# Performance work log

Measured on AMD Instinct MI355X. Metric: run time of the kernel, lower is better.

The kernel has to match this reference:

```python
import jax, jax.numpy as jnp
import numpy as np

NUM_HEADS = 8
NUM_GROUPS = 32
EPS = 1e-5


def group_norm(x, gamma, beta):
    # x: [B, C, H, W]; normalize over (C//G, H, W) within each of G groups
    B, C, H, W = x.shape
    xg = x.reshape(B, NUM_GROUPS, C // NUM_GROUPS, H, W)
    mean = xg.mean(axis=(2, 3, 4), keepdims=True)
    var = xg.var(axis=(2, 3, 4), keepdims=True)
    xn = ((xg - mean) * jax.lax.rsqrt(var + EPS)).reshape(B, C, H, W)
    return xn * gamma[None, :, None, None] + beta[None, :, None, None]


def setup_inputs() -> dict:
    key = jax.random.key(0)
    ks = jax.random.split(key, 7)
    B, C, H, W = 16, 512, 32, 32
    x = jax.random.normal(ks[0], (B, C, H, W), dtype=jnp.float32)
    gamma = jnp.ones((C,), dtype=jnp.float32)
    beta = jnp.zeros((C,), dtype=jnp.float32)
    # 1x1 convs == per-pixel linear layers
    w_qkv = jax.random.normal(ks[1], (3 * C, C), dtype=jnp.float32) * (1.0 / np.sqrt(C))
    b_qkv = jax.random.normal(ks[2], (3 * C,), dtype=jnp.float32) * 0.02
    w_proj = jax.random.normal(ks[3], (C, C), dtype=jnp.float32) * (1.0 / np.sqrt(C))
    b_proj = jax.random.normal(ks[4], (C,), dtype=jnp.float32) * 0.02
    return {"x": x, "gamma": gamma, "beta": beta, "w_qkv": w_qkv,
            "b_qkv": b_qkv, "w_proj": w_proj, "b_proj": b_proj}


def reference(x, gamma, beta, w_qkv, b_qkv, w_proj, b_proj):
    B, C, H, W = x.shape
    nh = NUM_HEADS
    d = C // nh
    N = H * W
    h = group_norm(x, gamma, beta)
    # 1x1 conv: [B,C,H,W] x [3C,C] -> [B,3C,H,W]
    qkv = jnp.einsum('bchw,oc->bohw', h, w_qkv) + b_qkv[None, :, None, None]
    qkv = qkv.reshape(B, 3, nh, d, N)  # matches torch reshape(B,3,heads,d,HW)
    q, k, v = qkv[:, 0], qkv[:, 1], qkv[:, 2]
    scale = d ** (-0.5)
    attn = jnp.einsum('bhdn,bhdm->bhnm', q, k) * scale  # [B,h,N,N]
    attn = jax.nn.softmax(attn, axis=-1)
    out = jnp.einsum('bhnm,bhdm->bhdn', attn, v)  # [B,h,d,N]
    out = out.reshape(B, C, H, W)
    proj = jnp.einsum('bchw,oc->bohw', out, w_proj) + b_proj[None, :, None, None]
    return x + proj
```

## Files before the change

kernel.cpp:

```cpp
#include <hip/hip_runtime.h>
#include <cstddef>

#define B_  16
#define C_  512
#define N_  1024

typedef __attribute__((ext_vector_type(8))) __bf16 bf16x8;
typedef __attribute__((ext_vector_type(4))) float f32x4;
typedef __attribute__((ext_vector_type(4))) short s16x4;

__device__ __forceinline__ unsigned short f2bf(float x) {
  unsigned u = __float_as_uint(x);
  return (unsigned short)((u + 0x7fffu + ((u >> 16) & 1u)) >> 16);
}
__device__ __forceinline__ float bf2f(unsigned short h) {
  return __uint_as_float(((unsigned)h) << 16);
}

#define GLDS16(g, l)                                                            \
  __builtin_amdgcn_global_load_lds(                                             \
      (const __attribute__((address_space(1))) void*)(g),                       \
      (__attribute__((address_space(3))) void*)(l), 16, 0, 0)

__global__ __launch_bounds__(256) void wconv_kernel(
    const float* __restrict__ wq, const float* __restrict__ wp,
    unsigned short* __restrict__ oq, unsigned short* __restrict__ op) {
  int i = blockIdx.x * 256 + threadIdx.x;
  const float4* src; unsigned short* dst; int off;
  if (i < 196608) { src = (const float4*)wq; dst = oq; off = i; }
  else            { src = (const float4*)wp; dst = op; off = i - 196608; }
  float4 v = src[off];
  union { unsigned short s[4]; ushort4 u; } o;
  o.s[0] = f2bf(v.x); o.s[1] = f2bf(v.y);
  o.s[2] = f2bf(v.z); o.s[3] = f2bf(v.w);
  *(ushort4*)(dst + (size_t)off * 4) = o.u;
}

__global__ __launch_bounds__(256) void gn_kernel(
    const float* __restrict__ x, const float* __restrict__ gamma,
    const float* __restrict__ beta, unsigned short* __restrict__ hT) {
  int bg = blockIdx.x;
  int b = bg >> 5, g = bg & 31;
  size_t base = ((size_t)b * C_ + (size_t)g * 16) * N_;
  const float4* x4 = (const float4*)(x + base);
  int tid = threadIdx.x;

  float sum = 0.f, sq = 0.f;
  float4 vv[16];
#pragma unroll
  for (int i = 0; i < 16; i++) {
    float4 v = x4[tid + i * 256];
    vv[i] = v;
    sum += v.x + v.y + v.z + v.w;
    sq  += v.x * v.x + v.y * v.y + v.z * v.z + v.w * v.w;
  }
#pragma unroll
  for (int off = 32; off > 0; off >>= 1) {
    sum += __shfl_down(sum, off, 64);
    sq  += __shfl_down(sq, off, 64);
  }
  __shared__ float sm[4], sv[4];
  int lane = tid & 63, w = tid >> 6;
  if (lane == 0) { sm[w] = sum; sv[w] = sq; }
  __syncthreads();
  if (tid == 0) {
    float s = sm[0] + sm[1] + sm[2] + sm[3];
    float q = sv[0] + sv[1] + sv[2] + sv[3];
    float mean = s * (1.f / 16384.f);
    float var  = q * (1.f / 16384.f) - mean * mean;
    sm[0] = mean;
    sv[0] = rsqrtf(var + 1e-5f);
  }
  __syncthreads();
  float mean = sm[0], rstd = sv[0];

  union { unsigned short s[16]; uint4 u[2]; } row[4];
#pragma unroll
  for (int i = 0; i < 16; i++) {
    int c = g * 16 + i;
    float ga = gamma[c] * rstd;
    float be = beta[c] - mean * ga;
    float4 v = vv[i];
    row[0].s[i] = f2bf(v.x * ga + be);
    row[1].s[i] = f2bf(v.y * ga + be);
    row[2].s[i] = f2bf(v.z * ga + be);
    row[3].s[i] = f2bf(v.w * ga + be);
  }
#pragma unroll
  for (int j = 0; j < 4; j++) {
    uint4* dst = (uint4*)(hT + ((size_t)b * N_ + 4 * tid + j) * C_ + g * 16);
    dst[0] = row[j].u[0];
    dst[1] = row[j].u[1];
  }
}

template <int OUT_BF16>
__global__ __launch_bounds__(256) void gemm_mfma(
    const unsigned short* __restrict__ Wb, const float* __restrict__ bias,
    const unsigned short* __restrict__ InT, const float* __restrict__ resid,
    void* __restrict__ Out, int M) {
  __shared__ __align__(16) unsigned short SH[4][128 * 34];

  const int b = blockIdx.z;
  const int n0 = blockIdx.x * 128, m0 = blockIdx.y * 128;
  const int tid = threadIdx.x;
  const int lane = tid & 63, wave = tid >> 6;
  const int col = lane & 15, quad = lane >> 4;
  const int wm = (wave >> 1) << 6, wn = (wave & 1) << 6;

  const unsigned short* Ag = Wb + (size_t)m0 * C_;
  const unsigned short* Bg = InT + ((size_t)b * N_ + n0) * C_;

  const int r0 = tid >> 2, c0 = (tid & 3) << 3;

  f32x4 acc[4][4];
#pragma unroll
  for (int i = 0; i < 4; i++)
#pragma unroll
    for (int j = 0; j < 4; j++) acc[i][j] = f32x4{0.f, 0.f, 0.f, 0.f};

  GLDS16(Ag + (size_t)r0 * C_ + c0,        &SH[0][tid * 8]);
  GLDS16(Ag + (size_t)(r0 + 64) * C_ + c0, &SH[0][(tid + 256) * 8]);
  GLDS16(Bg + (size_t)r0 * C_ + c0,        &SH[2][tid * 8]);
  GLDS16(Bg + (size_t)(r0 + 64) * C_ + c0, &SH[2][(tid + 256) * 8]);
  __syncthreads();

  for (int it = 0; it < 16; it++) {
    const int cur = it & 1;
    if (it < 15) {
      const int k1 = (it + 1) * 32;
      GLDS16(Ag + (size_t)r0 * C_ + k1 + c0,        &SH[cur ^ 1][tid * 8]);
      GLDS16(Ag + (size_t)(r0 + 64) * C_ + k1 + c0, &SH[cur ^ 1][(tid + 256) * 8]);
      GLDS16(Bg + (size_t)r0 * C_ + k1 + c0,        &SH[2 + (cur ^ 1)][tid * 8]);
      GLDS16(Bg + (size_t)(r0 + 64) * C_ + k1 + c0, &SH[2 + (cur ^ 1)][(tid + 256) * 8]);
    }

    bf16x8 af[4], bfr[4];
#pragma unroll
    for (int mt = 0; mt < 4; mt++)
      af[mt] = *(const bf16x8*)&SH[cur][(wm + mt * 16 + col) * 32 + quad * 8];
#pragma unroll
    for (int nt = 0; nt < 4; nt++)
      bfr[nt] = *(const bf16x8*)&SH[2 + cur][(wn + nt * 16 + col) * 32 + quad * 8];
#pragma unroll
    for (int mt = 0; mt < 4; mt++)
#pragma unroll
      for (int nt = 0; nt < 4; nt++)
        acc[mt][nt] = __builtin_amdgcn_mfma_f32_16x16x32_bf16(
            af[mt], bfr[nt], acc[mt][nt], 0, 0, 0);

    if (it < 15) __syncthreads();
  }

  const bool kT = OUT_BF16 && (m0 >= 512) && (m0 < 1024);

  if (kT) {
    unsigned short* epi = &SH[0][0];
    unsigned short* kt_out =
        (unsigned short*)Out + ((size_t)b * 1536 + 512) * N_ + (m0 - 512);
#pragma unroll
    for (int hf = 0; hf < 2; hf++) {
      __syncthreads();
      if ((wave & 1) == hf) {
#pragma unroll
        for (int mt = 0; mt < 4; mt++) {
          int mloc = wm + mt * 16 + quad * 4;
          int mabs = m0 + mloc;
#pragma unroll
          for (int nt = 0; nt < 4; nt++) {
            union { unsigned short s[4]; ushort4 v; } o;
#pragma unroll
            for (int r = 0; r < 4; r++)
              o.s[r] = f2bf(acc[mt][nt][r] + bias[mabs + r]);
            *(ushort4*)&epi[(nt * 16 + col) * 136 + mloc] = o.v;
          }
        }
      }
      __syncthreads();
#pragma unroll
      for (int pass = 0; pass < 4; pass++) {
        int n_l = (tid >> 4) + pass * 16;
        int ch = tid & 15;
        uint4 v = *(const uint4*)&epi[n_l * 136 + ch * 8];
        *(uint4*)(kt_out + (size_t)(n0 + hf * 64 + n_l) * 512 + ch * 8) = v;
      }
    }
    return;
  }

#pragma unroll
  for (int mt = 0; mt < 4; mt++) {
    int mbase = m0 + wm + mt * 16 + quad * 4;
#pragma unroll
    for (int nt = 0; nt < 4; nt++) {
      int n = n0 + wn + nt * 16 + col;
      if constexpr (OUT_BF16) {
#pragma unroll
        for (int r = 0; r < 4; r++) {
          float v = acc[mt][nt][r] + bias[mbase + r];
          ((unsigned short*)Out)[((size_t)b * M + mbase + r) * N_ + n] = f2bf(v);
        }
      } else {
#pragma unroll
        for (int r = 0; r < 4; r++) {
          int m = mbase + r;
          float v = acc[mt][nt][r] + bias[m];
          size_t off = ((size_t)b * M + m) * N_ + n;
          ((float*)Out)[off] = v + resid[off];
        }
      }
    }
  }
}

__device__ __forceinline__ void attn_tile(const bf16x8 (&qf)[2][2],
                                          const bf16x8 (&kf)[4][2],
                                          const s16x4 (&vf)[4][4],
                                          f32x4 (&O)[4][2], float (&l_i)[2]) {
#pragma unroll
  for (int nt = 0; nt < 2; nt++) {
    f32x4 sf[4];
#pragma unroll
    for (int mt = 0; mt < 4; mt++) sf[mt] = f32x4{0.f, 0.f, 0.f, 0.f};
    __builtin_amdgcn_s_setprio(1);
#pragma unroll
    for (int ks = 0; ks < 2; ks++)
#pragma unroll
      for (int mt = 0; mt < 4; mt++)
        sf[mt] = __builtin_amdgcn_mfma_f32_16x16x32_bf16(
            kf[mt][ks], qf[nt][ks], sf[mt], 0, 0, 0);
    __builtin_amdgcn_s_setprio(0);

    s16x4 pb[4];
    float lsum = 0.f;
#pragma unroll
    for (int kc = 0; kc < 4; kc++) {
      float e0 = __expf(sf[kc][0]);
      float e1 = __expf(sf[kc][1]);
      float e2 = __expf(sf[kc][2]);
      float e3 = __expf(sf[kc][3]);
      lsum += (e0 + e1) + (e2 + e3);
      unsigned lo = __builtin_amdgcn_perm(__float_as_uint(e1), __float_as_uint(e0), 0x07060302u);
      unsigned hi = __builtin_amdgcn_perm(__float_as_uint(e3), __float_as_uint(e2), 0x07060302u);
      union { unsigned u[2]; s16x4 v; } t;
      t.u[0] = lo; t.u[1] = hi;
      pb[kc] = t.v;
    }
    l_i[nt] += lsum;

    __builtin_amdgcn_s_setprio(1);
#pragma unroll
    for (int kc = 0; kc < 4; kc++)
#pragma unroll
      for (int mt = 0; mt < 4; mt++)
        O[mt][nt] = __builtin_amdgcn_mfma_f32_16x16x16bf16_1k(
            vf[mt][kc], pb[kc], O[mt][nt], 0, 0, 0);
    __builtin_amdgcn_s_setprio(0);
  }
}

template <int NB, int BOFF>
__global__ __launch_bounds__(256, 2) void attn_mfma(
    const unsigned short* __restrict__ qkv, unsigned short* __restrict__ aoT) {
  __shared__ __align__(16) unsigned short KtL[2][64 * 64];
  __shared__ __align__(16) unsigned short VsL[2][64 * 64];

  const int tid = threadIdx.x;
  const int wave = tid >> 6, lane = tid & 63;
  const int quad = lane >> 4, col = lane & 15;
  const int bi = blockIdx.x;
  const int hh = bi & 7;
  const int bq = bi >> 3;
  const int qb = bq / NB;
  const int b  = BOFF + (bq - qb * NB);
  const int qblk = qb * 128 + wave * 32;

  const unsigned short* qp  = qkv + ((size_t)b * 1536 + hh * 64) * N_;
  const unsigned short* ktp = qkv + ((size_t)b * 1536 + 512) * N_ + hh * 64;
  const unsigned short* vp  = qkv + ((size_t)b * 1536 + 1024 + hh * 64) * N_;

  const int sr = tid >> 3;
  const int sw8 = (((tid & 7) ^ (sr & 7)) << 3);

  bf16x8 qf[2][2];
#pragma unroll
  for (int nt = 0; nt < 2; nt++) {
    int qg = qblk + nt * 16 + col;
#pragma unroll
    for (int ks = 0; ks < 2; ks++) {
      union { unsigned short s[8]; bf16x8 v; } t;
#pragma unroll
      for (int j = 0; j < 8; j++) {
        int d = ks * 32 + quad * 8 + j;
        t.s[j] = f2bf(0.125f * bf2f(qp[(size_t)d * N_ + qg]));
      }
      qf[nt][ks] = t.v;
    }
  }

  float l_i[2];
  f32x4 O[4][2];
#pragma unroll
  for (int nt = 0; nt < 2; nt++) {
    l_i[nt] = 0.f;
#pragma unroll
    for (int mt = 0; mt < 4; mt++) O[mt][nt] = f32x4{0.f, 0.f, 0.f, 0.f};
  }

  {
    const unsigned short* kq = ktp + (size_t)sr * 512 + sw8;
    GLDS16(kq,                    &KtL[0][tid * 8]);
    GLDS16(kq + (size_t)32 * 512, &KtL[0][(256 + tid) * 8]);
    const unsigned short* vq = vp + (size_t)sr * N_ + sw8;
    GLDS16(vq,                    &VsL[0][tid * 8]);
    GLDS16(vq + (size_t)32 * N_,  &VsL[0][(256 + tid) * 8]);
  }
  __syncthreads();

  for (int kt = 0; kt < 16; kt++) {
    const int cur = kt & 1;
    if (kt < 15) {
      const unsigned short* kq = ktp + (size_t)((kt + 1) * 64 + sr) * 512 + sw8;
      GLDS16(kq,                    &KtL[cur ^ 1][tid * 8]);
      GLDS16(kq + (size_t)32 * 512, &KtL[cur ^ 1][(256 + tid) * 8]);
      const unsigned short* vq = vp + (size_t)sr * N_ + (kt + 1) * 64 + sw8;
      GLDS16(vq,                    &VsL[cur ^ 1][tid * 8]);
      GLDS16(vq + (size_t)32 * N_,  &VsL[cur ^ 1][(256 + tid) * 8]);
    }

    bf16x8 kf[4][2];
#pragma unroll
    for (int mt = 0; mt < 4; mt++) {
      int key = 16 * mt + col;
#pragma unroll
      for (int ks = 0; ks < 2; ks++)
        kf[mt][ks] = *(const bf16x8*)
            &KtL[cur][key * 64 + (((ks * 4 + quad) ^ (col & 7)) << 3)];
    }
    s16x4 vf[4][4];
#pragma unroll
    for (int mt = 0; mt < 4; mt++) {
      int d = 16 * mt + col;
#pragma unroll
      for (int kc = 0; kc < 4; kc++)
        vf[mt][kc] = *(const s16x4*)
            &VsL[cur][d * 64 + (((kc * 4 + quad) ^ ((col & 7) << 1)) << 2)];
    }

    attn_tile(qf, kf, vf, O, l_i);

    if (kt < 15) __syncthreads();
  }

#pragma unroll
  for (int nt = 0; nt < 2; nt++) {
    float ls = l_i[nt];
    ls += __shfl_xor(ls, 16, 64);
    ls += __shfl_xor(ls, 32, 64);
    float inv = 1.f / ls;
    int qg = qblk + nt * 16 + col;
    unsigned short* dst = aoT + ((size_t)b * N_ + qg) * C_ + hh * 64;
#pragma unroll
    for (int mt = 0; mt < 4; mt++) {
      union { unsigned short s[4]; ushort4 v; } o;
#pragma unroll
      for (int r = 0; r < 4; r++) o.s[r] = f2bf(O[mt][nt][r] * inv);
      *(ushort4*)(dst + mt * 16 + quad * 4) = o.v;
    }
  }
}

extern "C" void kernel_launch(void* const* d_in, const int* in_sizes, int n_in,
                              void* d_out, int out_size, void* d_ws, size_t ws_size,
                              hipStream_t stream) {
  (void)in_sizes; (void)n_in; (void)out_size; (void)ws_size;
  const float* x      = (const float*)d_in[0];
  const float* gamma  = (const float*)d_in[1];
  const float* beta   = (const float*)d_in[2];
  const float* w_qkv  = (const float*)d_in[3];
  const float* b_qkv  = (const float*)d_in[4];
  const float* w_proj = (const float*)d_in[5];
  const float* b_proj = (const float*)d_in[6];
  float* out = (float*)d_out;

  unsigned short* hT   = (unsigned short*)d_ws;
  unsigned short* qkvb = hT + (size_t)B_ * N_ * C_;
  unsigned short* aoT  = hT;
  unsigned short* wqb  = qkvb + (size_t)B_ * 1536 * N_;
  unsigned short* wpb  = wqb + (size_t)1536 * 512;

  wconv_kernel<<<dim3(1024), dim3(256), 0, stream>>>(w_qkv, w_proj, wqb, wpb);
  gn_kernel<<<dim3(B_ * 32), dim3(256), 0, stream>>>(x, gamma, beta, hT);
  gemm_mfma<1><<<dim3(8, 12, 16), dim3(256), 0, stream>>>(
      wqb, b_qkv, hT, (const float*)nullptr, (void*)qkvb, 1536);
  attn_mfma<12, 0><<<dim3(8 * 12 * 8), dim3(256), 0, stream>>>(qkvb, aoT);
  attn_mfma<4, 12><<<dim3(8 * 4 * 8), dim3(256), 0, stream>>>(qkvb, aoT);
  gemm_mfma<0><<<dim3(8, 4, 16), dim3(256), 0, stream>>>(
      wpb, b_proj, aoT, x, (void*)out, 512);
}
```

Baseline: 225.8 us.

## Split group-norm into stats and LDS-transposed normalize pass, rebalance attention launches

Group-norm statistics are now computed inside the weight-conversion kernel, which gains 512 extra blocks and writes mean and rstd to a workspace buffer. A separate normalize kernel re-reads x, then transposes through swizzled shared memory so each thread writes coalesced 16-byte rows of hT instead of strided per-channel stores. The attention work, previously split into a 12-batch launch and a 4-batch launch, now runs as four equal launches of four batches each. The change reads x twice and adds launches in exchange for better store coalescing and more even grids.

Result: slower. 262.0 us (+16.0%).

```diff
diff --git a/kernel.cpp b/kernel.cpp
--- a/kernel.cpp
+++ b/kernel.cpp
@@ -22,35 +22,30 @@
       (const __attribute__((address_space(1))) void*)(g),                       \
       (__attribute__((address_space(3))) void*)(l), 16, 0, 0)
 
-__global__ __launch_bounds__(256) void wconv_kernel(
+__global__ __launch_bounds__(256) void prep_kernel(
     const float* __restrict__ wq, const float* __restrict__ wp,
-    unsigned short* __restrict__ oq, unsigned short* __restrict__ op) {
-  int i = blockIdx.x * 256 + threadIdx.x;
-  const float4* src; unsigned short* dst; int off;
-  if (i < 196608) { src = (const float4*)wq; dst = oq; off = i; }
-  else            { src = (const float4*)wp; dst = op; off = i - 196608; }
-  float4 v = src[off];
-  union { unsigned short s[4]; ushort4 u; } o;
-  o.s[0] = f2bf(v.x); o.s[1] = f2bf(v.y);
-  o.s[2] = f2bf(v.z); o.s[3] = f2bf(v.w);
-  *(ushort4*)(dst + (size_t)off * 4) = o.u;
-}
-
-__global__ __launch_bounds__(256) void gn_kernel(
-    const float* __restrict__ x, const float* __restrict__ gamma,
-    const float* __restrict__ beta, unsigned short* __restrict__ hT) {
-  int bg = blockIdx.x;
+    unsigned short* __restrict__ oq, unsigned short* __restrict__ op,
+    const float* __restrict__ x, float* __restrict__ stats) {
+  int tid = threadIdx.x;
+  if (blockIdx.x < 1024) {
+    int i = blockIdx.x * 256 + tid;
+    const float4* src; unsigned short* dst; int off;
+    if (i < 196608) { src = (const float4*)wq; dst = oq; off = i; }
+    else            { src = (const float4*)wp; dst = op; off = i - 196608; }
+    float4 v = src[off];
+    union { unsigned short s[4]; ushort4 u; } o;
+    o.s[0] = f2bf(v.x); o.s[1] = f2bf(v.y);
+    o.s[2] = f2bf(v.z); o.s[3] = f2bf(v.w);
+    *(ushort4*)(dst + (size_t)off * 4) = o.u;
+    return;
+  }
+  int bg = blockIdx.x - 1024;
   int b = bg >> 5, g = bg & 31;
-  size_t base = ((size_t)b * C_ + (size_t)g * 16) * N_;
-  const float4* x4 = (const float4*)(x + base);
-  int tid = threadIdx.x;
-
+  const float4* x4 = (const float4*)(x + ((size_t)b * C_ + (size_t)g * 16) * N_);
   float sum = 0.f, sq = 0.f;
-  float4 vv[16];
 #pragma unroll
   for (int i = 0; i < 16; i++) {
     float4 v = x4[tid + i * 256];
-    vv[i] = v;
     sum += v.x + v.y + v.z + v.w;
     sq  += v.x * v.x + v.y * v.y + v.z * v.z + v.w * v.w;
   }
@@ -68,29 +63,57 @@
     float q = sv[0] + sv[1] + sv[2] + sv[3];
     float mean = s * (1.f / 16384.f);
     float var  = q * (1.f / 16384.f) - mean * mean;
-    sm[0] = mean;
-    sv[0] = rsqrtf(var + 1e-5f);
-  }
-  __syncthreads();
-  float mean = sm[0], rstd = sv[0];
-
-  union { unsigned short s[16]; uint4 u[2]; } row[4];
-#pragma unroll
-  for (int i = 0; i < 16; i++) {
-    int c = g * 16 + i;
-    float ga = gamma[c] * rstd;
-    float be = beta[c] - mean * ga;
-    float4 v = vv[i];
-    row[0].s[i] = f2bf(v.x * ga + be);
-    row[1].s[i] = f2bf(v.y * ga + be);
-    row[2].s[i] = f2bf(v.z * ga + be);
-    row[3].s[i] = f2bf(v.w * ga + be);
-  }
-#pragma unroll
-  for (int j = 0; j < 4; j++) {
-    uint4* dst = (uint4*)(hT + ((size_t)b * N_ + 4 * tid + j) * C_ + g * 16);
-    dst[0] = row[j].u[0];
-    dst[1] = row[j].u[1];
+    stats[bg * 2]     = mean;
+    stats[bg * 2 + 1] = rsqrtf(var + 1e-5f);
+  }
+}
+
+__global__ __launch_bounds__(256) void gn_norm(
+    const float* __restrict__ x, const float* __restrict__ gamma,
+    const float* __restrict__ beta, const float* __restrict__ stats,
+    unsigned short* __restrict__ hT) {
+  __shared__ __align__(16) unsigned short T[64][72];
+
+  const int bi = blockIdx.x;
+  const int nq = bi & 3, g4 = (bi >> 2) & 7, b = bi >> 5;
+  const int tid = threadIdx.x, lane = tid & 63, w = tid >> 6;
+  const int c0 = g4 * 64, n0 = nq * 256;
+  const int q = lane >> 4, n4 = lane & 15;
+
+  const int gidx = b * 32 + g4 * 4 + w;
+  const float mean = stats[gidx * 2], rstd = stats[gidx * 2 + 1];
+  float ga[4], be[4];
+#pragma unroll
+  for (int ri = 0; ri < 4; ri++) {
+    int c = w * 16 + q + ri * 4;
+    ga[ri] = gamma[c0 + c] * rstd;
+    be[ri] = beta[c0 + c] - mean * ga[ri];
+  }
+
+  const float* xb = x + ((size_t)b * C_ + c0) * N_ + n0;
+
+#pragma unroll
+  for (int s = 0; s < 4; s++) {
+#pragma unroll
+    for (int ri = 0; ri < 4; ri++) {
+      int c = w * 16 + q + ri * 4;
+      float4 v = *(const float4*)&xb[(size_t)c * N_ + s * 64 + n4 * 4];
+      int csw = c ^ ((n4 & 3) << 4);
+      T[n4 * 4 + 0][csw] = f2bf(v.x * ga[ri] + be[ri]);
+      T[n4 * 4 + 1][csw] = f2bf(v.y * ga[ri] + be[ri]);
+      T[n4 * 4 + 2][csw] = f2bf(v.z * ga[ri] + be[ri]);
+      T[n4 * 4 + 3][csw] = f2bf(v.w * ga[ri] + be[ri]);
+    }
+    __syncthreads();
+    {
+      int n_loc = tid >> 2, cc = (tid & 3) << 4;
+      int ccs = cc ^ (((n_loc >> 2) & 3) << 4);
+      const uint4* srcp = (const uint4*)&T[n_loc][ccs];
+      uint4* dst = (uint4*)&hT[((size_t)b * N_ + n0 + s * 64 + n_loc) * C_ + c0 + cc];
+      dst[0] = srcp[0];
+      dst[1] = srcp[1];
+    }
+    __syncthreads();
   }
 }
 
@@ -388,13 +411,16 @@
   unsigned short* aoT  = hT;
   unsigned short* wqb  = qkvb + (size_t)B_ * 1536 * N_;
   unsigned short* wpb  = wqb + (size_t)1536 * 512;
-
-  wconv_kernel<<<dim3(1024), dim3(256), 0, stream>>>(w_qkv, w_proj, wqb, wpb);
-  gn_kernel<<<dim3(B_ * 32), dim3(256), 0, stream>>>(x, gamma, beta, hT);
+  float* stats = (float*)(wpb + (size_t)512 * 512);
+
+  prep_kernel<<<dim3(1024 + 512), dim3(256), 0, stream>>>(w_qkv, w_proj, wqb, wpb, x, stats);
+  gn_norm<<<dim3(512), dim3(256), 0, stream>>>(x, gamma, beta, stats, hT);
   gemm_mfma<1><<<dim3(8, 12, 16), dim3(256), 0, stream>>>(
       wqb, b_qkv, hT, (const float*)nullptr, (void*)qkvb, 1536);
-  attn_mfma<12, 0><<<dim3(8 * 12 * 8), dim3(256), 0, stream>>>(qkvb, aoT);
-  attn_mfma<4, 12><<<dim3(8 * 4 * 8), dim3(256), 0, stream>>>(qkvb, aoT);
+  attn_mfma<4, 0><<<dim3(256), dim3(256), 0, stream>>>(qkvb, aoT);
+  attn_mfma<4, 4><<<dim3(256), dim3(256), 0, stream>>>(qkvb, aoT);
+  attn_mfma<4, 8><<<dim3(256), dim3(256), 0, stream>>>(qkvb, aoT);
+  attn_mfma<4, 12><<<dim3(256), dim3(256), 0, stream>>>(qkvb, aoT);
   gemm_mfma<0><<<dim3(8, 4, 16), dim3(256), 0, stream>>>(
       wpb, b_proj, aoT, x, (void*)out, 512);
 }
```
